# Kernel optimization log

Hardware: AMD Instinct MI355X
Metric: run time of the kernel (lower is better)

The kernel has to match this reference:

```python
import jax, jax.numpy as jnp
import numpy as np

N_L = 100000   # local nodes
N_V = 1000     # virtual nodes
D_IN = 64
H = 64         # hidden_channels
D_OUT = 32
E_LL = 1000000
E_LV = 100000
E_VV = 50000


def setup_inputs() -> dict:
    key = jax.random.key(0)
    ks = jax.random.split(key, 16)
    s_in = 1.0 / np.sqrt(D_IN)   # fan-in init scale
    s_h = 1.0 / np.sqrt(H)
    return {
        "x_local": jax.random.normal(ks[0], (N_L, D_IN), jnp.float32),
        "x_virtual": jax.random.normal(ks[1], (N_V, D_IN), jnp.float32),
        # GCNConv (local->local): weight + bias
        "W_gcn": jax.random.normal(ks[2], (D_IN, H), jnp.float32) * s_in,
        "b_gcn": jnp.zeros((H,), jnp.float32),
        # SAGEConv (local->virtual): lin_l (neighbor agg, with bias), lin_r (root)
        "Wl_lv": jax.random.normal(ks[3], (D_IN, H), jnp.float32) * s_in,
        "Wr_lv": jax.random.normal(ks[4], (D_IN, H), jnp.float32) * s_in,
        "b_lv": jnp.zeros((H,), jnp.float32),
        # SAGEConv (virtual->virtual)
        "Wl_vv": jax.random.normal(ks[5], (D_IN, H), jnp.float32) * s_in,
        "Wr_vv": jax.random.normal(ks[6], (D_IN, H), jnp.float32) * s_in,
        "b_vv": jnp.zeros((H,), jnp.float32),
        # final Linear(hidden -> dim_out)
        "W_lin": jax.random.normal(ks[7], (H, D_OUT), jnp.float32) * s_h,
        "b_lin": jnp.zeros((D_OUT,), jnp.float32),
        # edge indices
        "edge_ll": jax.random.randint(ks[8], (2, E_LL), 0, N_L),
        "edge_lv_src": jax.random.randint(ks[9], (E_LV,), 0, N_L),
        "edge_lv_dst": jax.random.randint(ks[10], (E_LV,), 0, N_V),
        "edge_vv": jax.random.randint(ks[11], (2, E_VV), 0, N_V),
    }


def _gcn_conv(x, W, b, row, col, n):
    # gcn_norm with add_self_loops=False: deg from dst (col), sym norm
    ones = jnp.ones(row.shape[0], x.dtype)
    deg = jax.ops.segment_sum(ones, col, num_segments=n)
    dinv = jnp.where(deg > 0, jax.lax.rsqrt(jnp.maximum(deg, 1.0)), 0.0)
    norm = dinv[row] * dinv[col]                      # [E]
    h = x @ W                                         # [n,H]
    msg = h[row] * norm[:, None]                      # [E,H] gather
    return jax.ops.segment_sum(msg, col, num_segments=n) + b


def _sage_conv(x_src, x_dst, Wl, Wr, b, src, dst, n_dst):
    # mean aggregation of source features over in-edges
    agg = jax.ops.segment_sum(x_src[src], dst, num_segments=n_dst)
    cnt = jax.ops.segment_sum(jnp.ones(src.shape[0], x_src.dtype), dst,
                              num_segments=n_dst)
    agg = agg / jnp.maximum(cnt, 1.0)[:, None]
    return agg @ Wl + b + x_dst @ Wr


def reference(x_local, x_virtual, W_gcn, b_gcn, Wl_lv, Wr_lv, b_lv,
              Wl_vv, Wr_vv, b_vv, W_lin, b_lin,
              edge_ll, edge_lv_src, edge_lv_dst, edge_vv):
    # HeteroConv layer (sum-aggregate outputs per destination node type)
    out_ll = _gcn_conv(x_local, W_gcn, b_gcn, edge_ll[0], edge_ll[1], N_L)
    out_lv = _sage_conv(x_local, x_virtual, Wl_lv, Wr_lv, b_lv,
                        edge_lv_src, edge_lv_dst, N_V)
    out_vv = _sage_conv(x_virtual, x_virtual, Wl_vv, Wr_vv, b_vv,
                        edge_vv[0], edge_vv[1], N_V)
    h_local = jax.nn.relu(out_ll)
    h_virtual = jax.nn.relu(out_lv + out_vv)  # sum across relations -> relu
    del h_virtual  # only 'local' feeds the final linear head
    return h_local @ W_lin + b_lin
```

## Files before the change

kernel.cpp:

```cpp
#include <hip/hip_runtime.h>

#define N_L 100000
#define N_V 1000
#define D_IN 64
#define HCH 64
#define D_OUT 32
#define E_LL 1000000

#define NCLS 8
#define DST_PER_CLS 12500
#define NBLK1 1024
#define BCAP 256
#define GW 400
#define HW 200
#define NSB 32
#define NGSB 256
#define SUBCAP 4608
#define SORTCAP 2560
#define SCSTRIDE 16

#define L2CAP 384
#define L2THR 128
#define BINSUB_BPC 64
#define SLABS (NBLK1 / BINSUB_BPC)

typedef unsigned int uint32;
typedef unsigned long long u64;
typedef __attribute__((ext_vector_type(8))) short bfx8;
typedef __attribute__((ext_vector_type(4))) float f32x4;
typedef __attribute__((ext_vector_type(4))) float fvec4;
typedef __attribute__((ext_vector_type(4))) unsigned short usvec4;

__device__ inline float bf2f(unsigned short u) {
    return __uint_as_float(((uint32)u) << 16);
}
__device__ inline unsigned short f2bf(float f) {
    uint32 u = __float_as_uint(f);
    u = (u + 0x7fffu + ((u >> 16) & 1u)) >> 16;
    return (unsigned short)u;
}
__device__ inline void bar_lds() {
    asm volatile("s_waitcnt lgkmcnt(0)\n\ts_barrier" ::: "memory");
}

__global__ __launch_bounds__(256) void binclass_kernel(
    const int* __restrict__ row, const int* __restrict__ col,
    int* __restrict__ classcnt, uint32* __restrict__ classpairs)
{
    __shared__ uint32 sbin[NCLS][BCAP];
    __shared__ int scnt[NCLS];
    if (threadIdx.x < NCLS) scnt[threadIdx.x] = 0;
    bar_lds();

    const int blk = blockIdx.x;
    const int per = (E_LL + NBLK1 - 1) / NBLK1;
    const int beg = blk * per;
    const int end = (beg + per < E_LL) ? beg + per : E_LL;
    const int lane = threadIdx.x & 63;
    const int wv = threadIdx.x >> 6;

    for (int i0 = beg; i0 < end; i0 += 256) {
        int i = i0 + threadIdx.x;
        if (i < end) {
            int c = col[i];
            int r = row[i];
            int cls = c / DST_PER_CLS;
            uint32 pack = ((uint32)r << 14) | (uint32)(c - cls * DST_PER_CLS);
            u64 act = __ballot(1);
            u64 b0 = __ballot(cls & 1);
            u64 b1 = __ballot(cls & 2);
            u64 b2 = __ballot(cls & 4);
            u64 mask = ((cls & 1) ? b0 : ~b0) & ((cls & 2) ? b1 : ~b1)
                     & ((cls & 4) ? b2 : ~b2) & act;
            int leader = __ffsll(mask) - 1;
            int rank = __popcll(mask & ((1ull << lane) - 1ull));
            int base = 0;
            if (lane == leader) base = atomicAdd(&scnt[cls], __popcll(mask));
            base = __shfl(base, leader);
            int slot = base + rank;
            if (slot < BCAP) sbin[cls][slot] = pack;
        }
    }
    bar_lds();
    for (int b = wv; b < NCLS; b += 4) {
        int cnt = scnt[b]; if (cnt > BCAP) cnt = BCAP;
        uint32* dst = classpairs + ((size_t)b * NBLK1 + blk) * BCAP;
        for (int k = lane; k < cnt; k += 64) dst[k] = sbin[b][k];
        if (lane == 0) classcnt[b * NBLK1 + blk] = cnt;
    }
}

__global__ __launch_bounds__(256) void binsub_kernel(
    const int* __restrict__ classcnt, const uint32* __restrict__ classpairs,
    int* __restrict__ subcur, uint32* __restrict__ subpairs)
{
    __shared__ uint32 sbin[NSB][L2CAP];
    __shared__ int scnt[NSB];
    if (threadIdx.x < NSB) scnt[threadIdx.x] = 0;
    bar_lds();

    const int cls = blockIdx.x / BINSUB_BPC;
    const int chunk = blockIdx.x % BINSUB_BPC;
    const int s0 = chunk * SLABS;
    const int lane = threadIdx.x & 63;
    const int wv = threadIdx.x >> 6;

    for (int s = s0; s < s0 + SLABS; ++s) {
        int len = classcnt[cls * NBLK1 + s];
        const uint32* cp = classpairs + ((size_t)cls * NBLK1 + s) * BCAP;
        if (threadIdx.x < len) {
            uint32 p = cp[threadIdx.x];
            int c_lo = (int)(p & 16383u);
            uint32 r = p >> 14;
            int sb = c_lo / GW;
            uint32 pack = (r << 9) | (uint32)(c_lo - sb * GW);
            u64 act = __ballot(1);
            u64 b0 = __ballot(sb & 1);
            u64 b1 = __ballot(sb & 2);
            u64 b2 = __ballot(sb & 4);
            u64 b3 = __ballot(sb & 8);
            u64 b4 = __ballot(sb & 16);
            u64 mask = ((sb & 1) ? b0 : ~b0) & ((sb & 2) ? b1 : ~b1)
                     & ((sb & 4) ? b2 : ~b2) & ((sb & 8) ? b3 : ~b3)
                     & ((sb & 16) ? b4 : ~b4) & act;
            int leader = __ffsll(mask) - 1;
            int rank = __popcll(mask & ((1ull << lane) - 1ull));
            int base = 0;
            if (lane == leader) base = atomicAdd(&scnt[sb], __popcll(mask));
            base = __shfl(base, leader);
            sbin[sb][base + rank] = pack;
        }
        bar_lds();
        for (int b = wv; b < NSB; b += 4) {
            int cnt = scnt[b];
            if (cnt >= L2THR) {
                int gb;
                int gsb = cls * NSB + b;
                if (lane == 0) gb = atomicAdd(&subcur[gsb * SCSTRIDE], cnt);
                gb = __shfl(gb, 0);
                uint32* dst = subpairs + (size_t)gsb * SUBCAP;
                for (int k = lane; k < cnt; k += 64)
                    if (gb + k < SUBCAP) dst[gb + k] = sbin[b][k];
                if (lane == 0) scnt[b] = 0;
            }
        }
        bar_lds();
    }
    for (int b = wv; b < NSB; b += 4) {
        int cnt = scnt[b];
        if (cnt > 0) {
            int gb;
            int gsb = cls * NSB + b;
            if (lane == 0) gb = atomicAdd(&subcur[gsb * SCSTRIDE], cnt);
            gb = __shfl(gb, 0);
            uint32* dst = subpairs + (size_t)gsb * SUBCAP;
            for (int k = lane; k < cnt; k += 64)
                if (gb + k < SUBCAP) dst[gb + k] = sbin[b][k];
        }
    }
}

__global__ __launch_bounds__(512) void degdinv_kernel(
    const uint32* __restrict__ subpairs, const int* __restrict__ subcur,
    float* __restrict__ dinv, int* __restrict__ rptrg)
{
    __shared__ int hcnt[512];
    __shared__ int scn[512];
    const int gsb = blockIdx.x;
    const int cls = gsb >> 5;
    const int sb = gsb & 31;
    const int lo = cls * DST_PER_CLS + sb * GW;
    int w = DST_PER_CLS - sb * GW; if (w > GW) w = GW;
    const int tid = threadIdx.x;

    hcnt[tid] = 0;
    bar_lds();
    int cnt = subcur[gsb * SCSTRIDE]; if (cnt > SUBCAP) cnt = SUBCAP;
    const uint32* sp = subpairs + (size_t)gsb * SUBCAP;
    for (int i = tid; i < cnt; i += 512)
        atomicAdd(&hcnt[sp[i] & 511u], 1);
    bar_lds();

    int v = hcnt[tid];
    scn[tid] = v;
    bar_lds();
    for (int ofs = 1; ofs < 512; ofs <<= 1) {
        int add = (tid >= ofs) ? scn[tid - ofs] : 0;
        bar_lds();
        scn[tid] += add;
        bar_lds();
    }
    rptrg[gsb * 512 + tid] = scn[tid] - v;
    if (tid < w)
        dinv[lo + tid] = (v > 0) ? rsqrtf((float)v) : 0.0f;
}

__global__ void xbconv_kernel(const float* __restrict__ x,
                              const float* __restrict__ dinv,
                              unsigned short* __restrict__ xb) {
    int n4 = N_L * D_IN / 4;
    int idx = blockIdx.x * blockDim.x + threadIdx.x;
    int stride = gridDim.x * blockDim.x;
    for (; idx < n4; idx += stride) {
        fvec4 v = ((const fvec4*)x)[idx];
        float d = dinv[idx >> 4];
        usvec4 o;
        o.x = f2bf(v.x * d);
        o.y = f2bf(v.y * d);
        o.z = f2bf(v.z * d);
        o.w = f2bf(v.w * d);
        ((usvec4*)xb)[idx] = o;
    }
}

__global__ __launch_bounds__(512) void gather_epi_kernel(
    const unsigned short* __restrict__ xb,
    const uint32* __restrict__ subpairs, const int* __restrict__ subcur,
    const int* __restrict__ rptrg,
    const float* __restrict__ Wg, const float* __restrict__ bg,
    const float* __restrict__ Wl, const float* __restrict__ bl,
    float* __restrict__ out)
{
    extern __shared__ char smem[];
    unsigned short* hacc  = (unsigned short*)smem;
    unsigned short* hbufp = (unsigned short*)(smem + 29952);
    uint32* sorted = (uint32*)(smem + 48384);
    int* rptr_l = (int*)(smem + 58624);
    int* cur    = (int*)(smem + 59456);

    const int gsb = blockIdx.x >> 1;
    const int hb  = blockIdx.x & 1;
    const int cls = gsb >> 5;
    const int sb  = gsb & 31;
    const int lo_bin = cls * DST_PER_CLS + sb * GW;
    int wbin = DST_PER_CLS - sb * GW; if (wbin > GW) wbin = GW;
    const int lo_node = hb * HW;
    int w = wbin - lo_node; if (w > HW) w = HW; if (w < 0) w = 0;
    const int lo = lo_bin + lo_node;

    const int tid = threadIdx.x;
    const int lane = tid & 63;
    const int wv = tid >> 6;

    int cnt = subcur[gsb * SCSTRIDE]; if (cnt > SUBCAP) cnt = SUBCAP;
    const uint32* sp = subpairs + (size_t)gsb * SUBCAP;
    const int* rg = rptrg + gsb * 512;

    const int base0 = rg[lo_node];
    if (tid <= w) {
        int rl = rg[lo_node + tid] - base0;
        rptr_l[tid] = rl;
        if (tid < w) cur[tid] = rl;
    }
    bar_lds();

    for (int i = tid; i < cnt; i += 512) {
        uint32 p = sp[i];
        int cl = (int)(p & 511u) - lo_node;
        if (cl >= 0 && cl < w) {
            int pos = atomicAdd(&cur[cl], 1);
            if (pos < SORTCAP) sorted[pos] = p >> 9;
        }
    }
    bar_lds();

    for (int c = wv; c < w; c += 8) {
        int s = rptr_l[c], e = rptr_l[c + 1];
        if (e > SORTCAP) e = SORTCAP;
        int cntc = e - s;
        float a0 = 0.f, a1 = 0.f, a2 = 0.f, a3 = 0.f;
        float a4 = 0.f, a5 = 0.f, a6 = 0.f, a7 = 0.f;
        int j = s;
        for (; j + 8 <= e; j += 8) {
            int r0 = sorted[j], r1 = sorted[j + 1];
            int r2 = sorted[j + 2], r3 = sorted[j + 3];
            int r4 = sorted[j + 4], r5 = sorted[j + 5];
            int r6 = sorted[j + 6], r7 = sorted[j + 7];
            a0 += bf2f(xb[(size_t)r0 * D_IN + lane]);
            a1 += bf2f(xb[(size_t)r1 * D_IN + lane]);
            a2 += bf2f(xb[(size_t)r2 * D_IN + lane]);
            a3 += bf2f(xb[(size_t)r3 * D_IN + lane]);
            a4 += bf2f(xb[(size_t)r4 * D_IN + lane]);
            a5 += bf2f(xb[(size_t)r5 * D_IN + lane]);
            a6 += bf2f(xb[(size_t)r6 * D_IN + lane]);
            a7 += bf2f(xb[(size_t)r7 * D_IN + lane]);
        }
        for (; j < e; ++j) {
            int r = sorted[j];
            a0 += bf2f(xb[(size_t)r * D_IN + lane]);
        }
        float dv = (cntc > 0) ? rsqrtf((float)cntc) : 0.0f;
        float s01 = (a0 + a1) + (a2 + a3);
        float s23 = (a4 + a5) + (a6 + a7);
        hacc[c * 72 + lane] = f2bf((s01 + s23) * dv);
    }
    bar_lds();

    if (w == 0) return;

    const int lm = lane & 15, lg = lane >> 4, kseg = lg * 8;

    bfx8 wg0[4], wg1[4], wl0[2], wl1[2];
    #pragma unroll
    for (int n = 0; n < 4; ++n) {
        #pragma unroll
        for (int jj = 0; jj < 8; ++jj) {
            wg0[n][jj] = (short)f2bf(Wg[(kseg + jj) * HCH + n * 16 + lm]);
            wg1[n][jj] = (short)f2bf(Wg[(32 + kseg + jj) * HCH + n * 16 + lm]);
        }
    }
    #pragma unroll
    for (int n = 0; n < 2; ++n) {
        #pragma unroll
        for (int jj = 0; jj < 8; ++jj) {
            wl0[n][jj] = (short)f2bf(Wl[(kseg + jj) * D_OUT + n * 16 + lm]);
            wl1[n][jj] = (short)f2bf(Wl[(32 + kseg + jj) * D_OUT + n * 16 + lm]);
        }
    }
    float bgv[4], blv[2];
    #pragma unroll
    for (int n = 0; n < 4; ++n) bgv[n] = bg[n * 16 + lm];
    #pragma unroll
    for (int n = 0; n < 2; ++n) blv[n] = bl[n * 16 + lm];

    const int ntile = (w + 15) >> 4;
    for (int t = wv; t < ntile; t += 8) {
        const int m0 = t * 16;
        const int arow = m0 + lm;
        const unsigned short* fr = hacc + arow * 72;
        bfx8 a0 = *(const bfx8*)(fr + kseg);
        bfx8 a1 = *(const bfx8*)(fr + 32 + kseg);

        unsigned short* hbw = hbufp + wv * (16 * 72);
        #pragma unroll
        for (int n = 0; n < 4; ++n) {
            f32x4 cacc = {0.0f, 0.0f, 0.0f, 0.0f};
            cacc = __builtin_amdgcn_mfma_f32_16x16x32_bf16(a0, wg0[n], cacc, 0, 0, 0);
            cacc = __builtin_amdgcn_mfma_f32_16x16x32_bf16(a1, wg1[n], cacc, 0, 0, 0);
            #pragma unroll
            for (int i = 0; i < 4; ++i) {
                float h = fmaxf(cacc[i] + bgv[n], 0.0f);
                hbw[(lg * 4 + i) * 72 + n * 16 + lm] = f2bf(h);
            }
        }
        bfx8 a20 = *(const bfx8*)(hbw + lm * 72 + kseg);
        bfx8 a21 = *(const bfx8*)(hbw + lm * 72 + 32 + kseg);

        #pragma unroll
        for (int n2 = 0; n2 < 2; ++n2) {
            f32x4 d = {0.0f, 0.0f, 0.0f, 0.0f};
            d = __builtin_amdgcn_mfma_f32_16x16x32_bf16(a20, wl0[n2], d, 0, 0, 0);
            d = __builtin_amdgcn_mfma_f32_16x16x32_bf16(a21, wl1[n2], d, 0, 0, 0);
            #pragma unroll
            for (int i = 0; i < 4; ++i) {
                int mrow = m0 + lg * 4 + i;
                if (mrow < w)
                    out[(size_t)(lo + mrow) * D_OUT + n2 * 16 + lm] = d[i] + blv[n2];
            }
        }
    }
}

extern "C" void kernel_launch(void* const* d_in, const int* in_sizes, int n_in,
                              void* d_out, int out_size, void* d_ws, size_t ws_size,
                              hipStream_t stream) {
    const float* x_local = (const float*)d_in[0];
    const float* W_gcn   = (const float*)d_in[2];
    const float* b_gcn   = (const float*)d_in[3];
    const float* W_lin   = (const float*)d_in[10];
    const float* b_lin   = (const float*)d_in[11];
    const int*   edge_ll = (const int*)d_in[12];
    const int*   row = edge_ll;
    const int*   col = edge_ll + E_LL;

    char* base = (char*)d_ws;
    int*    subcur     = (int*)(base + 0);
    int*    classcnt   = (int*)(base + 16384);
    float*  dinvp      = (float*)(base + 49152);
    int*    rptrg      = (int*)(base + 449536);
    uint32* classpairs = (uint32*)(base + 973824);
    uint32* subpairs   = (uint32*)(base + 9362432);
    unsigned short* xb = (unsigned short*)(base + 14081024);
    float* out = (float*)d_out;

    (void)hipMemsetAsync(base, 0, 16384, stream);

    binclass_kernel<<<NBLK1, 256, 0, stream>>>(row, col, classcnt, classpairs);
    binsub_kernel<<<NCLS * BINSUB_BPC, 256, 0, stream>>>(
        classcnt, classpairs, subcur, subpairs);
    degdinv_kernel<<<NGSB, 512, 0, stream>>>(subpairs, subcur, dinvp, rptrg);
    xbconv_kernel<<<2048, 256, 0, stream>>>(x_local, dinvp, xb);
    gather_epi_kernel<<<2 * NGSB, 512, 60416, stream>>>(
        xb, subpairs, subcur, rptrg, W_gcn, b_gcn, W_lin, b_lin, out);
}
```

Before: 112.2 us.

## Balance gather work across waves by edge ranges and compute CSR offsets locally

The row-pointer prefix scan moves out of the degree kernel into the gather kernel, so the global rptrg buffer and its round trip through memory go away. The gather loop also changes from one destination node per wave to an even split of the sorted edge list across the 8 waves, with node ids packed next to the source ids. Partial sums at range boundaries go to shared memory and are merged by wave 0. This targets load imbalance from uneven degrees, at the cost of an extra histogram pass, per-edge branch checks, a serial fixup step and more LDS per block (65856 bytes), which may reduce occupancy.

```diff
diff --git a/kernel.cpp b/kernel.cpp
--- a/kernel.cpp
+++ b/kernel.cpp
@@ -162,37 +162,26 @@
 
 __global__ __launch_bounds__(512) void degdinv_kernel(
     const uint32* __restrict__ subpairs, const int* __restrict__ subcur,
-    float* __restrict__ dinv, int* __restrict__ rptrg)
+    float* __restrict__ dinv)
 {
     __shared__ int hcnt[512];
-    __shared__ int scn[512];
     const int gsb = blockIdx.x;
     const int cls = gsb >> 5;
     const int sb = gsb & 31;
     const int lo = cls * DST_PER_CLS + sb * GW;
     int w = DST_PER_CLS - sb * GW; if (w > GW) w = GW;
-    const int tid = threadIdx.x;
-
-    hcnt[tid] = 0;
+
+    hcnt[threadIdx.x] = 0;
     bar_lds();
     int cnt = subcur[gsb * SCSTRIDE]; if (cnt > SUBCAP) cnt = SUBCAP;
     const uint32* sp = subpairs + (size_t)gsb * SUBCAP;
-    for (int i = tid; i < cnt; i += 512)
+    for (int i = threadIdx.x; i < cnt; i += 512)
         atomicAdd(&hcnt[sp[i] & 511u], 1);
     bar_lds();
-
-    int v = hcnt[tid];
-    scn[tid] = v;
-    bar_lds();
-    for (int ofs = 1; ofs < 512; ofs <<= 1) {
-        int add = (tid >= ofs) ? scn[tid - ofs] : 0;
-        bar_lds();
-        scn[tid] += add;
-        bar_lds();
-    }
-    rptrg[gsb * 512 + tid] = scn[tid] - v;
-    if (tid < w)
-        dinv[lo + tid] = (v > 0) ? rsqrtf((float)v) : 0.0f;
+    if (threadIdx.x < w) {
+        int d = hcnt[threadIdx.x];
+        dinv[lo + threadIdx.x] = (d > 0) ? rsqrtf((float)d) : 0.0f;
+    }
 }
 
 __global__ void xbconv_kernel(const float* __restrict__ x,
@@ -216,7 +205,6 @@
 __global__ __launch_bounds__(512) void gather_epi_kernel(
     const unsigned short* __restrict__ xb,
     const uint32* __restrict__ subpairs, const int* __restrict__ subcur,
-    const int* __restrict__ rptrg,
     const float* __restrict__ Wg, const float* __restrict__ bg,
     const float* __restrict__ Wl, const float* __restrict__ bl,
     float* __restrict__ out)
@@ -225,8 +213,11 @@
     unsigned short* hacc  = (unsigned short*)smem;
     unsigned short* hbufp = (unsigned short*)(smem + 29952);
     uint32* sorted = (uint32*)(smem + 48384);
-    int* rptr_l = (int*)(smem + 58624);
-    int* cur    = (int*)(smem + 59456);
+    int* hist  = (int*)(smem + 58624);
+    int* scn   = (int*)(smem + 59648);
+    int* cur   = (int*)(smem + 60672);
+    float* bpart = (float*)(smem + 61696);
+    int* bnode = (int*)(smem + 65792);
 
     const int gsb = blockIdx.x >> 1;
     const int hb  = blockIdx.x & 1;
@@ -244,14 +235,31 @@
 
     int cnt = subcur[gsb * SCSTRIDE]; if (cnt > SUBCAP) cnt = SUBCAP;
     const uint32* sp = subpairs + (size_t)gsb * SUBCAP;
-    const int* rg = rptrg + gsb * 512;
-
-    const int base0 = rg[lo_node];
-    if (tid <= w) {
-        int rl = rg[lo_node + tid] - base0;
-        rptr_l[tid] = rl;
-        if (tid < w) cur[tid] = rl;
-    }
+
+    {
+        uint32* hz = (uint32*)hacc;
+        for (int i = tid; i < 208 * 36; i += 512) hz[i] = 0u;
+        if (tid < 256) hist[tid] = 0;
+        if (tid < 16) bnode[tid] = -1;
+    }
+    bar_lds();
+
+    for (int i = tid; i < cnt; i += 512) {
+        int cl = (int)(sp[i] & 511u) - lo_node;
+        if (cl >= 0 && cl < w) atomicAdd(&hist[cl], 1);
+    }
+    bar_lds();
+
+    int v = (tid < 256) ? hist[tid] : 0;
+    if (tid < 256) scn[tid] = v;
+    bar_lds();
+    for (int ofs = 1; ofs < 256; ofs <<= 1) {
+        int add = (tid < 256 && tid >= ofs) ? scn[tid - ofs] : 0;
+        bar_lds();
+        if (tid < 256) scn[tid] += add;
+        bar_lds();
+    }
+    if (tid < 256) cur[tid] = scn[tid] - v;
     bar_lds();
 
     for (int i = tid; i < cnt; i += 512) {
@@ -259,40 +267,84 @@
         int cl = (int)(p & 511u) - lo_node;
         if (cl >= 0 && cl < w) {
             int pos = atomicAdd(&cur[cl], 1);
-            if (pos < SORTCAP) sorted[pos] = p >> 9;
-        }
-    }
-    bar_lds();
-
-    for (int c = wv; c < w; c += 8) {
-        int s = rptr_l[c], e = rptr_l[c + 1];
-        if (e > SORTCAP) e = SORTCAP;
-        int cntc = e - s;
-        float a0 = 0.f, a1 = 0.f, a2 = 0.f, a3 = 0.f;
-        float a4 = 0.f, a5 = 0.f, a6 = 0.f, a7 = 0.f;
-        int j = s;
-        for (; j + 8 <= e; j += 8) {
-            int r0 = sorted[j], r1 = sorted[j + 1];
-            int r2 = sorted[j + 2], r3 = sorted[j + 3];
-            int r4 = sorted[j + 4], r5 = sorted[j + 5];
-            int r6 = sorted[j + 6], r7 = sorted[j + 7];
-            a0 += bf2f(xb[(size_t)r0 * D_IN + lane]);
-            a1 += bf2f(xb[(size_t)r1 * D_IN + lane]);
-            a2 += bf2f(xb[(size_t)r2 * D_IN + lane]);
-            a3 += bf2f(xb[(size_t)r3 * D_IN + lane]);
-            a4 += bf2f(xb[(size_t)r4 * D_IN + lane]);
-            a5 += bf2f(xb[(size_t)r5 * D_IN + lane]);
-            a6 += bf2f(xb[(size_t)r6 * D_IN + lane]);
-            a7 += bf2f(xb[(size_t)r7 * D_IN + lane]);
-        }
-        for (; j < e; ++j) {
-            int r = sorted[j];
-            a0 += bf2f(xb[(size_t)r * D_IN + lane]);
-        }
-        float dv = (cntc > 0) ? rsqrtf((float)cntc) : 0.0f;
-        float s01 = (a0 + a1) + (a2 + a3);
-        float s23 = (a4 + a5) + (a6 + a7);
-        hacc[c * 72 + lane] = f2bf((s01 + s23) * dv);
+            if (pos < SORTCAP) sorted[pos] = ((p >> 9) << 8) | (uint32)cl;
+        }
+    }
+    bar_lds();
+
+    int ch = scn[255]; if (ch > SORTCAP) ch = SORTCAP;
+    {
+        int a = (ch * wv) >> 3;
+        int b = (ch * (wv + 1)) >> 3;
+        if (a < b) {
+            float acc = 0.0f;
+            int curn = (int)(sorted[a] & 255u);
+            bool firstopen = true;
+
+#define GSTEP(EK, VK)                                                        \
+            {                                                                \
+                int nk = (int)((EK) & 255u);                                 \
+                if (nk != curn) {                                            \
+                    if (firstopen) {                                         \
+                        bpart[(2 * wv) * 64 + lane] = acc;                   \
+                        if (lane == 0) bnode[2 * wv] = curn;                 \
+                        firstopen = false;                                   \
+                    } else {                                                 \
+                        hacc[curn * 72 + lane] =                             \
+                            f2bf(acc * rsqrtf((float)hist[curn]));           \
+                    }                                                        \
+                    acc = 0.0f; curn = nk;                                   \
+                }                                                            \
+                acc += (VK);                                                 \
+            }
+
+            int j = a;
+            for (; j + 8 <= b; j += 8) {
+                uint32 e0 = sorted[j + 0], e1 = sorted[j + 1];
+                uint32 e2 = sorted[j + 2], e3 = sorted[j + 3];
+                uint32 e4 = sorted[j + 4], e5 = sorted[j + 5];
+                uint32 e6 = sorted[j + 6], e7 = sorted[j + 7];
+                float v0 = bf2f(xb[(size_t)(e0 >> 8) * D_IN + lane]);
+                float v1 = bf2f(xb[(size_t)(e1 >> 8) * D_IN + lane]);
+                float v2 = bf2f(xb[(size_t)(e2 >> 8) * D_IN + lane]);
+                float v3 = bf2f(xb[(size_t)(e3 >> 8) * D_IN + lane]);
+                float v4 = bf2f(xb[(size_t)(e4 >> 8) * D_IN + lane]);
+                float v5 = bf2f(xb[(size_t)(e5 >> 8) * D_IN + lane]);
+                float v6 = bf2f(xb[(size_t)(e6 >> 8) * D_IN + lane]);
+                float v7 = bf2f(xb[(size_t)(e7 >> 8) * D_IN + lane]);
+                GSTEP(e0, v0) GSTEP(e1, v1) GSTEP(e2, v2) GSTEP(e3, v3)
+                GSTEP(e4, v4) GSTEP(e5, v5) GSTEP(e6, v6) GSTEP(e7, v7)
+            }
+            for (; j < b; ++j) {
+                uint32 e = sorted[j];
+                float vv = bf2f(xb[(size_t)(e >> 8) * D_IN + lane]);
+                GSTEP(e, vv)
+            }
+#undef GSTEP
+            if (firstopen) {
+                bpart[(2 * wv) * 64 + lane] = acc;
+                if (lane == 0) bnode[2 * wv] = curn;
+            } else {
+                bpart[(2 * wv + 1) * 64 + lane] = acc;
+                if (lane == 0) bnode[2 * wv + 1] = curn;
+            }
+        }
+    }
+    bar_lds();
+
+    if (wv == 0) {
+        for (int e2 = 0; e2 < 16; ++e2) {
+            int n = bnode[e2];
+            if (n < 0) continue;
+            bool first = true;
+            for (int f = 0; f < e2; ++f)
+                if (bnode[f] == n) { first = false; break; }
+            if (!first) continue;
+            float s = bpart[e2 * 64 + lane];
+            for (int f = e2 + 1; f < 16; ++f)
+                if (bnode[f] == n) s += bpart[f * 64 + lane];
+            hacc[n * 72 + lane] = f2bf(s * rsqrtf((float)hist[n]));
+        }
     }
     bar_lds();
 
@@ -377,10 +429,9 @@
     int*    subcur     = (int*)(base + 0);
     int*    classcnt   = (int*)(base + 16384);
     float*  dinvp      = (float*)(base + 49152);
-    int*    rptrg      = (int*)(base + 449536);
-    uint32* classpairs = (uint32*)(base + 973824);
-    uint32* subpairs   = (uint32*)(base + 9362432);
-    unsigned short* xb = (unsigned short*)(base + 14081024);
+    uint32* classpairs = (uint32*)(base + 449536);
+    uint32* subpairs   = (uint32*)(base + 8838144);
+    unsigned short* xb = (unsigned short*)(base + 13556736);
     float* out = (float*)d_out;
 
     (void)hipMemsetAsync(base, 0, 16384, stream);
@@ -388,8 +439,8 @@
     binclass_kernel<<<NBLK1, 256, 0, stream>>>(row, col, classcnt, classpairs);
     binsub_kernel<<<NCLS * BINSUB_BPC, 256, 0, stream>>>(
         classcnt, classpairs, subcur, subpairs);
-    degdinv_kernel<<<NGSB, 512, 0, stream>>>(subpairs, subcur, dinvp, rptrg);
+    degdinv_kernel<<<NGSB, 512, 0, stream>>>(subpairs, subcur, dinvp);
     xbconv_kernel<<<2048, 256, 0, stream>>>(x_local, dinvp, xb);
-    gather_epi_kernel<<<2 * NGSB, 512, 60416, stream>>>(
-        xb, subpairs, subcur, rptrg, W_gcn, b_gcn, W_lin, b_lin, out);
-}
+    gather_epi_kernel<<<2 * NGSB, 512, 65856, stream>>>(
+        xb, subpairs, subcur, W_gcn, b_gcn, W_lin, b_lin, out);
+}
```

After: 100.7 us. 10.3% less time.
